# Performance work log

Hardware: AMD Instinct MI355X
Metric: run time of the kernel (lower is better)

The kernel has to match this reference:

```python
import jax, jax.numpy as jnp
import numpy as np

N_NODES = 50000
N_EDGES = 800000
IN_DIM = 128
HID = 128
HEADS = 4
OUT_DIM = 32
NEG_SLOPE = 0.2  # DGL GATConv default


def _gat_params(key, in_dim, out_feat, heads):
    k1, k2, k3 = jax.random.split(key, 3)
    s = 1.0 / np.sqrt(in_dim)
    W = jax.random.normal(k1, (in_dim, heads * out_feat), jnp.float32) * s
    attn_l = jax.random.normal(k2, (heads, out_feat), jnp.float32) * 0.1
    attn_r = jax.random.normal(k3, (heads, out_feat), jnp.float32) * 0.1
    b = jnp.zeros((heads * out_feat,), jnp.float32)
    return W, attn_l, attn_r, b


def setup_inputs() -> dict:
    key = jax.random.key(0)
    ks = jax.random.split(key, 10)
    inp = {
        "x_am": jax.random.normal(ks[0], (N_NODES, IN_DIM), jnp.float32),
        "x_ph": jax.random.normal(ks[1], (N_NODES, IN_DIM), jnp.float32),
        "exist": jax.random.uniform(ks[2], (N_EDGES,), jnp.float32),
        "am_exist": jax.random.uniform(ks[3], (N_EDGES,), jnp.float32),
        "src": jax.random.randint(ks[4], (N_EDGES,), 0, N_NODES, jnp.int32),
        "dst": jax.random.randint(ks[5], (N_EDGES,), 0, N_NODES, jnp.int32),
    }
    # layer 0 (input_dim -> hidden//head per head), layer 1 (hidden -> output_dim per head)
    inp["W0a"], inp["al0a"], inp["ar0a"], inp["b0a"] = _gat_params(ks[6], IN_DIM, HID // HEADS, HEADS)
    inp["W0p"], inp["al0p"], inp["ar0p"], inp["b0p"] = _gat_params(ks[7], IN_DIM, HID // HEADS, HEADS)
    inp["W1a"], inp["al1a"], inp["ar1a"], inp["b1a"] = _gat_params(ks[8], HID, OUT_DIM, HEADS)
    inp["W1p"], inp["al1p"], inp["ar1p"], inp["b1p"] = _gat_params(ks[9], HID, OUT_DIM, HEADS)
    return inp


def gat_conv(x, src, dst, W, attn_l, attn_r, b, edge_w, n_nodes):
    """DGL-style GATConv with edge_weight: out[i] = sum_{e: dst=i} softmax_i(LeakyReLU(el[src]+er[dst])) * w_e * ft[src]."""
    heads, outf = attn_l.shape
    ft = (x @ W).reshape(-1, heads, outf)                 # (N, H, F)
    el = jnp.sum(ft * attn_l, axis=-1)                    # (N, H)
    er = jnp.sum(ft * attn_r, axis=-1)                    # (N, H)
    e = jax.nn.leaky_relu(el[src] + er[dst], NEG_SLOPE)   # (E, H)
    emax = jax.ops.segment_max(e, dst, num_segments=n_nodes)
    emax = jnp.where(jnp.isfinite(emax), emax, 0.0)       # guard isolated nodes
    ex = jnp.exp(e - emax[dst])
    denom = jax.ops.segment_sum(ex, dst, num_segments=n_nodes)
    a = ex / jnp.maximum(denom[dst], 1e-9)                # edge softmax over incoming edges
    a = a * edge_w[:, None]                               # post-softmax edge weighting
    out = jax.ops.segment_sum(ft[src] * a[:, :, None], dst, num_segments=n_nodes)  # (N, H, F)
    return out + b.reshape(heads, outf)


def reference(x_am, x_ph, exist, am_exist,
              W0a, al0a, ar0a, b0a, W0p, al0p, ar0p, b0p,
              W1a, al1a, ar1a, b1a, W1p, al1p, ar1p, b1p,
              src, dst):
    n = x_am.shape[0]
    # layer 0: GATConv -> flatten -> ReLU (dropout rate 0 in eval)
    h_am = gat_conv(x_am, src, dst, W0a, al0a, ar0a, b0a, am_exist, n)
    h_ph = gat_conv(x_ph, src, dst, W0p, al0p, ar0p, b0p, exist, n)
    h_am = jax.nn.relu(h_am.reshape(n, -1))
    h_ph = jax.nn.relu(h_ph.reshape(n, -1))
    # layer 1 (last): GATConv -> mean over heads
    h_am = gat_conv(h_am, src, dst, W1a, al1a, ar1a, b1a, am_exist, n).mean(axis=1)
    h_ph = gat_conv(h_ph, src, dst, W1p, al1p, ar1p, b1p, exist, n).mean(axis=1)
    return (h_am, h_ph)
```

## Files before the change

kernel.cpp:

```cpp
#include <hip/hip_runtime.h>
#include <hip/hip_fp16.h>


typedef _Float16 f16x8 __attribute__((ext_vector_type(8)));
typedef float f32x4 __attribute__((ext_vector_type(4)));

struct GemmP { const void* X; const __half* Wt; const float *al, *ar; __half* Y; float *el, *er; };
struct ChP   { const __half* ft; const float *el, *er, *bias; void* out; };

__global__ void hist_kernel(const int* __restrict__ dst, int* __restrict__ counts, int E) {
  int e = blockIdx.x * blockDim.x + threadIdx.x;
  if (e < E) atomicAdd(&counts[dst[e]], 1);
}

__global__ __launch_bounds__(256) void scan1_kernel(const int* __restrict__ counts,
                                                    int* __restrict__ incl,
                                                    int* __restrict__ bsum, int n) {
  __shared__ int lds[256];
  int i = blockIdx.x * 256 + threadIdx.x;
  int v = (i < n) ? counts[i] : 0;
  lds[threadIdx.x] = v;
  __syncthreads();
  for (int off = 1; off < 256; off <<= 1) {
    int t = (threadIdx.x >= off) ? lds[threadIdx.x - off] : 0;
    __syncthreads();
    lds[threadIdx.x] += t;
    __syncthreads();
  }
  if (i < n) incl[i] = lds[threadIdx.x];
  if (threadIdx.x == 255) bsum[blockIdx.x] = lds[255];
}

__global__ __launch_bounds__(256) void scan2_kernel(int* __restrict__ bsum, int nb) {
  __shared__ int lds[256];
  int carry = 0;
  for (int base = 0; base < nb; base += 256) {
    int i = base + threadIdx.x;
    int v = (i < nb) ? bsum[i] : 0;
    lds[threadIdx.x] = v;
    __syncthreads();
    for (int off = 1; off < 256; off <<= 1) {
      int t = (threadIdx.x >= off) ? lds[threadIdx.x - off] : 0;
      __syncthreads();
      lds[threadIdx.x] += t;
      __syncthreads();
    }
    if (i < nb) bsum[i] = carry + lds[threadIdx.x] - v;
    carry += lds[255];
    __syncthreads();
  }
}

__global__ void scan3_kernel(const int* __restrict__ counts, const int* __restrict__ incl,
                             const int* __restrict__ bsum_ex, int* __restrict__ offsets,
                             int n, int E) {
  int i = blockIdx.x * blockDim.x + threadIdx.x;
  if (i < n) offsets[i] = incl[i] - counts[i] + bsum_ex[i >> 8];
  if (i == 0) offsets[n] = E;
}

__global__ void fill_kernel(const int* __restrict__ src, const int* __restrict__ dst,
                            const float* __restrict__ exist, const float* __restrict__ am_exist,
                            int* __restrict__ cursor, int4* __restrict__ edge16, int E) {
  int e = blockIdx.x * blockDim.x + threadIdx.x;
  if (e >= E) return;
  int pos = atomicAdd(&cursor[dst[e]], 1);
  edge16[pos] = make_int4(src[e], __float_as_int(am_exist[e]), __float_as_int(exist[e]), 0);
}

__global__ void wprep_kernel(const float* __restrict__ W0a, const float* __restrict__ W0p,
                             const float* __restrict__ W1a, const float* __restrict__ W1p,
                             __half* __restrict__ Wt) {
  int m = blockIdx.y;
  const float* W = (m == 0) ? W0a : (m == 1) ? W0p : (m == 2) ? W1a : W1p;
  __half* O = Wt + (size_t)m * 16384;
  int i = blockIdx.x * 256 + threadIdx.x;
  int nn = i >> 7, k = i & 127;
  O[nn * 128 + k] = __float2half_rn(W[k * 128 + nn]);
}

template <int AFP16>
__global__ __launch_bounds__(256) void gemm_kernel(GemmP p0, GemmP p1, int n) {
  GemmP p = blockIdx.y ? p1 : p0;
  constexpr int LDH = 72;
  constexpr int LDE = 136;
  __shared__ __half lds[2 * 128 * LDH];
  __half* As = lds;
  __half* Ws = lds + 128 * LDH;
  int t = threadIdx.x;
  int row0 = blockIdx.x << 7;
  int wv = t >> 6, lane = t & 63;
  int m = lane & 15, q = lane >> 4;

  f32x4 acc[2][8];
#pragma unroll
  for (int rt = 0; rt < 2; ++rt)
#pragma unroll
    for (int ct = 0; ct < 8; ++ct) acc[rt][ct] = (f32x4){0.f, 0.f, 0.f, 0.f};

#pragma unroll
  for (int kh = 0; kh < 2; ++kh) {
    __syncthreads();
    if (AFP16) {
      const __half* Xh = (const __half*)p.X;
#pragma unroll
      for (int i = 0; i < 4; ++i) {
        int c = t + (i << 8);
        int r = c >> 3, o8 = c & 7;
        uint4 v = make_uint4(0, 0, 0, 0);
        if (row0 + r < n)
          v = *(const uint4*)(Xh + (size_t)(row0 + r) * 128 + (kh << 6) + (o8 << 3));
        *(uint4*)(As + r * LDH + (o8 << 3)) = v;
      }
    } else {
      const float* Xf = (const float*)p.X;
#pragma unroll
      for (int i = 0; i < 8; ++i) {
        int c = t + (i << 8);
        int r = c >> 4, f4 = c & 15;
        float4 v = make_float4(0.f, 0.f, 0.f, 0.f);
        if (row0 + r < n)
          v = *(const float4*)(Xf + (size_t)(row0 + r) * 128 + (kh << 6) + (f4 << 2));
        union { __half h[4]; uint2 u; } pk;
        pk.h[0] = __float2half_rn(v.x); pk.h[1] = __float2half_rn(v.y);
        pk.h[2] = __float2half_rn(v.z); pk.h[3] = __float2half_rn(v.w);
        *(uint2*)(As + r * LDH + (f4 << 2)) = pk.u;
      }
    }
#pragma unroll
    for (int i = 0; i < 4; ++i) {
      int c = t + (i << 8);
      int r = c >> 3, o8 = c & 7;
      uint4 v = *(const uint4*)(p.Wt + (size_t)r * 128 + (kh << 6) + (o8 << 3));
      *(uint4*)(Ws + r * LDH + (o8 << 3)) = v;
    }
    __syncthreads();
#pragma unroll
    for (int kc = 0; kc < 2; ++kc) {
      f16x8 a0 = *(const f16x8*)(As + (wv * 32 + m) * LDH + kc * 32 + q * 8);
      f16x8 a1 = *(const f16x8*)(As + (wv * 32 + 16 + m) * LDH + kc * 32 + q * 8);
#pragma unroll
      for (int ct = 0; ct < 8; ++ct) {
        f16x8 b = *(const f16x8*)(Ws + (ct * 16 + m) * LDH + kc * 32 + q * 8);
        acc[0][ct] = __builtin_amdgcn_mfma_f32_16x16x32_f16(a0, b, acc[0][ct], 0, 0, 0);
        acc[1][ct] = __builtin_amdgcn_mfma_f32_16x16x32_f16(a1, b, acc[1][ct], 0, 0, 0);
      }
    }
  }
  __syncthreads();
#pragma unroll
  for (int rt = 0; rt < 2; ++rt) {
    int rbase = wv * 32 + rt * 16 + q * 4;
#pragma unroll
    for (int ct = 0; ct < 8; ++ct) {
      int col = ct * 16 + m;
#pragma unroll
      for (int r = 0; r < 4; ++r)
        lds[(rbase + r) * LDE + col] = __float2half_rn(acc[rt][ct][r]);
    }
  }
  __syncthreads();
  {
    int r = t & 127;
    int half = t >> 7;
    int row = row0 + r;
    if (row < n) {
      float e0 = 0.f, e1 = 0.f, r0 = 0.f, r1 = 0.f;
#pragma unroll
      for (int i = 0; i < 8; ++i) {
        int cbase = half * 64 + i * 8;
        f16x8 v = *(const f16x8*)(lds + r * LDE + cbase);
        *(uint4*)(p.Y + (size_t)row * 128 + cbase) = *(const uint4*)&v;
#pragma unroll
        for (int j = 0; j < 8; ++j) {
          float f = (float)v[j];
          float av = p.al[cbase + j];
          float rv = p.ar[cbase + j];
          if (((i * 8 + j) >> 5) == 0) { e0 = fmaf(f, av, e0); r0 = fmaf(f, rv, r0); }
          else                         { e1 = fmaf(f, av, e1); r1 = fmaf(f, rv, r1); }
        }
      }
      *(float2*)(p.el + (size_t)row * 4 + half * 2) = make_float2(e0, e1);
      *(float2*)(p.er + (size_t)row * 4 + half * 2) = make_float2(r0, r1);
    }
  }
}

template <int LAYER>
__global__ __launch_bounds__(256) void gather_kernel(ChP c0, ChP c1,
                                                     const int* __restrict__ offs,
                                                     const int4* __restrict__ edge16, int n) {
  int t = threadIdx.x;
  int w = t >> 6;
  int lane = t & 63;
  int node = blockIdx.x * 2 + (w >> 1);
  int ch = w & 1;
  if (node >= n) return;
  ChP P = ch ? c1 : c0;
  int hh = lane >> 4;

  int start = __builtin_amdgcn_readfirstlane(offs[node]);
  int end = __builtin_amdgcn_readfirstlane(offs[node + 1]);
  float er_h = P.er[(size_t)node * 4 + hh];
  const __half2* ftbase = (const __half2*)P.ft;
  const float* elbase = P.el;

  float acc0 = 0.f, acc1 = 0.f, l = 0.f;
  int k = start;
  while (k + 8 <= end) {
    int4 ed[8];
#pragma unroll
    for (int j = 0; j < 8; ++j) ed[j] = edge16[k + j];
#pragma unroll
    for (int j = 0; j < 8; ++j) {
      int s = ed[j].x;
      float wgt = __int_as_float(ch ? ed[j].z : ed[j].y);
      float elv = (elbase + (size_t)s * 4)[hh];
      float2 f = __half22float2((ftbase + (size_t)s * 64)[lane]);
      float e = elv + er_h;
      e = (e > 0.f) ? e : 0.2f * e;
      float x = __expf(e);
      l += x;
      float cv = x * wgt;
      acc0 = fmaf(cv, f.x, acc0);
      acc1 = fmaf(cv, f.y, acc1);
    }
    k += 8;
  }
  for (; k < end; ++k) {
    int4 ed = edge16[k];
    int s = ed.x;
    float wgt = __int_as_float(ch ? ed.z : ed.y);
    float elv = (elbase + (size_t)s * 4)[hh];
    float2 f = __half22float2((ftbase + (size_t)s * 64)[lane]);
    float e = elv + er_h;
    e = (e > 0.f) ? e : 0.2f * e;
    float x = __expf(e);
    l += x;
    float cv = x * wgt;
    acc0 = fmaf(cv, f.x, acc0);
    acc1 = fmaf(cv, f.y, acc1);
  }

  float rl = 1.f / fmaxf(l, 1e-9f);
  float2 b2 = *(const float2*)(P.bias + lane * 2);
  float v0 = fmaf(acc0, rl, b2.x);
  float v1 = fmaf(acc1, rl, b2.y);
  if (LAYER == 0) {
    __half2 h = __floats2half2_rn(fmaxf(v0, 0.f), fmaxf(v1, 0.f));
    ((__half2*)P.out)[(size_t)node * 64 + lane] = h;
  } else {
    v0 += __shfl_xor(v0, 16); v1 += __shfl_xor(v1, 16);
    v0 += __shfl_xor(v0, 32); v1 += __shfl_xor(v1, 32);
    if (lane < 16) {
      *(float2*)((float*)P.out + (size_t)node * 32 + lane * 2) =
          make_float2(0.25f * v0, 0.25f * v1);
    }
  }
}

extern "C" void kernel_launch(void* const* d_in, const int* in_sizes, int n_in,
                              void* d_out, int out_size, void* d_ws, size_t ws_size,
                              hipStream_t stream) {
  const float* x_am = (const float*)d_in[0];
  const float* x_ph = (const float*)d_in[1];
  const float* exist = (const float*)d_in[2];
  const float* am_exist = (const float*)d_in[3];
  const int* src = (const int*)d_in[4];
  const int* dst = (const int*)d_in[5];
  const float* W0a = (const float*)d_in[6];
  const float* al0a = (const float*)d_in[7];
  const float* ar0a = (const float*)d_in[8];
  const float* b0a = (const float*)d_in[9];
  const float* W0p = (const float*)d_in[10];
  const float* al0p = (const float*)d_in[11];
  const float* ar0p = (const float*)d_in[12];
  const float* b0p = (const float*)d_in[13];
  const float* W1a = (const float*)d_in[14];
  const float* al1a = (const float*)d_in[15];
  const float* ar1a = (const float*)d_in[16];
  const float* b1a = (const float*)d_in[17];
  const float* W1p = (const float*)d_in[18];
  const float* al1p = (const float*)d_in[19];
  const float* ar1p = (const float*)d_in[20];
  const float* b1p = (const float*)d_in[21];

  int n = in_sizes[0] / 128;
  int E = in_sizes[2];
  int N_pad = (n + 255) & ~255;
  int nb = (n + 255) / 256;
  int NB_pad = (nb + 63) & ~63;

  size_t szN = (size_t)N_pad * 4;
  size_t szOffs = (size_t)(N_pad + 8) * 4;
  size_t szE16 = (size_t)E * 16;
  size_t szFt16 = (size_t)n * 128 * 2;
  size_t szEl = (size_t)N_pad * 4 * 4;
  size_t szWt = (size_t)4 * 128 * 128 * 2;

  auto rnd = [](size_t b) { return (b + 255) & ~(size_t)255; };
  size_t fixed = 3 * rnd(szN) + rnd((size_t)NB_pad * 4) + rnd(szOffs) + rnd(szE16) +
                 4 * rnd(szEl) + rnd(szWt);
  bool dual = ws_size >= fixed + 4 * rnd(szFt16);

  char* p = (char*)d_ws;
  auto take = [&](size_t b) { char* q = p; p += (b + 255) & ~(size_t)255; return q; };
  int* counts = (int*)take(szN);
  int* cursor = (int*)take(szN);
  int* incl = (int*)take(szN);
  int* bsum = (int*)take((size_t)NB_pad * 4);
  int* offs = (int*)take(szOffs);
  int4* edge16 = (int4*)take(szE16);
  __half* Wt = (__half*)take(szWt);
  float* el_am = (float*)take(szEl);
  float* el_ph = (float*)take(szEl);
  float* er_am = (float*)take(szEl);
  float* er_ph = (float*)take(szEl);
  __half* ft_am = (__half*)take(szFt16);
  __half* ft_ph = dual ? (__half*)take(szFt16) : ft_am;
  __half* hb_am = (__half*)take(szFt16);
  __half* hb_ph = dual ? (__half*)take(szFt16) : hb_am;

  float* out_am = (float*)d_out;
  float* out_ph = out_am + (size_t)n * 32;

  hipMemsetAsync(counts, 0, szN, stream);
  hist_kernel<<<(E + 255) / 256, 256, 0, stream>>>(dst, counts, E);
  wprep_kernel<<<dim3(64, 4), 256, 0, stream>>>(W0a, W0p, W1a, W1p, Wt);
  scan1_kernel<<<nb, 256, 0, stream>>>(counts, incl, bsum, n);
  scan2_kernel<<<1, 256, 0, stream>>>(bsum, nb);
  scan3_kernel<<<nb, 256, 0, stream>>>(counts, incl, bsum, offs, n, E);
  hipMemcpyAsync(cursor, offs, szN, hipMemcpyDeviceToDevice, stream);
  fill_kernel<<<(E + 255) / 256, 256, 0, stream>>>(src, dst, exist, am_exist,
                                                   cursor, edge16, E);

  int gg = (n + 127) / 128;
  int gw = (n + 1) / 2;
  GemmP g0a{x_am, Wt,          al0a, ar0a, ft_am, el_am, er_am};
  GemmP g0p{x_ph, Wt + 16384,  al0p, ar0p, ft_ph, el_ph, er_ph};
  GemmP g1a{hb_am, Wt + 32768, al1a, ar1a, ft_am, el_am, er_am};
  GemmP g1p{hb_ph, Wt + 49152, al1p, ar1p, ft_ph, el_ph, er_ph};
  ChP c0a{ft_am, el_am, er_am, b0a, hb_am};
  ChP c0p{ft_ph, el_ph, er_ph, b0p, hb_ph};
  ChP c1a{ft_am, el_am, er_am, b1a, out_am};
  ChP c1p{ft_ph, el_ph, er_ph, b1p, out_ph};

  if (dual) {
    gemm_kernel<0><<<dim3(gg, 2), 256, 0, stream>>>(g0a, g0p, n);
    gather_kernel<0><<<gw, 256, 0, stream>>>(c0a, c0p, offs, edge16, n);
    gemm_kernel<1><<<dim3(gg, 2), 256, 0, stream>>>(g1a, g1p, n);
    gather_kernel<1><<<gw, 256, 0, stream>>>(c1a, c1p, offs, edge16, n);
  } else {
    gemm_kernel<0><<<dim3(gg, 2), 256, 0, stream>>>(g0a, g0a, n);
    gather_kernel<0><<<gw, 256, 0, stream>>>(c0a, c0a, offs, edge16, n);
    gemm_kernel<1><<<dim3(gg, 2), 256, 0, stream>>>(g1a, g1a, n);
    gather_kernel<1><<<gw, 256, 0, stream>>>(c1a, c1a, offs, edge16, n);
    gemm_kernel<0><<<dim3(gg, 2), 256, 0, stream>>>(g0p, g0p, n);
    gather_kernel<0><<<gw, 256, 0, stream>>>(c0p, c0p, offs, edge16, n);
    gemm_kernel<1><<<dim3(gg, 2), 256, 0, stream>>>(g1p, g1p, n);
    gather_kernel<1><<<gw, 256, 0, stream>>>(c1p, c1p, offs, edge16, n);
  }
}
```

Before: 433.8 us.

## Precompute per-edge attention exponentials in a separate edge-parallel kernel

Adds a coef_kernel that, for every CSR-sorted edge, computes exp(leaky_relu(el[src]+er[dst])) for all four heads of both channels and stores them as float4 arrays. The gather kernel then reads these coalesced per-edge values instead of doing a random el[src] load and an exp per lane per edge. To support this, dst is stored in the edge record, and scan3 writes the cursor directly, which removes the device-to-device memcpy. The cost is an extra kernel per layer and about 25 MB of extra write and read traffic for the coefficient arrays.

After: 433.5 us. Within noise of the previous version (-0.1%).

```diff
diff --git a/kernel.cpp b/kernel.cpp
--- a/kernel.cpp
+++ b/kernel.cpp
@@ -6,7 +6,8 @@
 typedef float f32x4 __attribute__((ext_vector_type(4)));
 
 struct GemmP { const void* X; const __half* Wt; const float *al, *ar; __half* Y; float *el, *er; };
-struct ChP   { const __half* ft; const float *el, *er, *bias; void* out; };
+struct ChP   { const __half* ft; const float* X; const float* bias; void* out; };
+struct CoefP { const float *el, *er; float* X; };
 
 __global__ void hist_kernel(const int* __restrict__ dst, int* __restrict__ counts, int E) {
   int e = blockIdx.x * blockDim.x + threadIdx.x;
@@ -53,9 +54,13 @@
 
 __global__ void scan3_kernel(const int* __restrict__ counts, const int* __restrict__ incl,
                              const int* __restrict__ bsum_ex, int* __restrict__ offsets,
-                             int n, int E) {
+                             int* __restrict__ cursor, int n, int E) {
   int i = blockIdx.x * blockDim.x + threadIdx.x;
-  if (i < n) offsets[i] = incl[i] - counts[i] + bsum_ex[i >> 8];
+  if (i < n) {
+    int v = incl[i] - counts[i] + bsum_ex[i >> 8];
+    offsets[i] = v;
+    cursor[i] = v;
+  }
   if (i == 0) offsets[n] = E;
 }
 
@@ -64,8 +69,9 @@
                             int* __restrict__ cursor, int4* __restrict__ edge16, int E) {
   int e = blockIdx.x * blockDim.x + threadIdx.x;
   if (e >= E) return;
-  int pos = atomicAdd(&cursor[dst[e]], 1);
-  edge16[pos] = make_int4(src[e], __float_as_int(am_exist[e]), __float_as_int(exist[e]), 0);
+  int d = dst[e];
+  int pos = atomicAdd(&cursor[d], 1);
+  edge16[pos] = make_int4(src[e], d, __float_as_int(am_exist[e]), __float_as_int(exist[e]));
 }
 
 __global__ void wprep_kernel(const float* __restrict__ W0a, const float* __restrict__ W0p,
@@ -186,6 +192,36 @@
   }
 }
 
+__global__ __launch_bounds__(256) void coef_kernel(CoefP a, CoefP b,
+                                                   const int4* __restrict__ edge16, int E) {
+  int e = blockIdx.x * 256 + threadIdx.x;
+  if (e >= E) return;
+  int4 r = edge16[e];
+  int s = r.x, d = r.y;
+  {
+    float4 el = *(const float4*)(a.el + (size_t)s * 4);
+    float4 er = *(const float4*)(a.er + (size_t)d * 4);
+    float4 x;
+    float v;
+    v = el.x + er.x; v = (v > 0.f) ? v : 0.2f * v; x.x = __expf(v);
+    v = el.y + er.y; v = (v > 0.f) ? v : 0.2f * v; x.y = __expf(v);
+    v = el.z + er.z; v = (v > 0.f) ? v : 0.2f * v; x.z = __expf(v);
+    v = el.w + er.w; v = (v > 0.f) ? v : 0.2f * v; x.w = __expf(v);
+    *(float4*)(a.X + (size_t)e * 4) = x;
+  }
+  {
+    float4 el = *(const float4*)(b.el + (size_t)s * 4);
+    float4 er = *(const float4*)(b.er + (size_t)d * 4);
+    float4 x;
+    float v;
+    v = el.x + er.x; v = (v > 0.f) ? v : 0.2f * v; x.x = __expf(v);
+    v = el.y + er.y; v = (v > 0.f) ? v : 0.2f * v; x.y = __expf(v);
+    v = el.z + er.z; v = (v > 0.f) ? v : 0.2f * v; x.z = __expf(v);
+    v = el.w + er.w; v = (v > 0.f) ? v : 0.2f * v; x.w = __expf(v);
+    *(float4*)(b.X + (size_t)e * 4) = x;
+  }
+}
+
 template <int LAYER>
 __global__ __launch_bounds__(256) void gather_kernel(ChP c0, ChP c1,
                                                      const int* __restrict__ offs,
@@ -201,9 +237,8 @@
 
   int start = __builtin_amdgcn_readfirstlane(offs[node]);
   int end = __builtin_amdgcn_readfirstlane(offs[node + 1]);
-  float er_h = P.er[(size_t)node * 4 + hh];
   const __half2* ftbase = (const __half2*)P.ft;
-  const float* elbase = P.el;
+  const float* Xb = P.X;
 
   float acc0 = 0.f, acc1 = 0.f, l = 0.f;
   int k = start;
@@ -211,35 +246,33 @@
     int4 ed[8];
 #pragma unroll
     for (int j = 0; j < 8; ++j) ed[j] = edge16[k + j];
+    const float* Xk = Xb + (size_t)k * 4;
+    float xs[8];
+#pragma unroll
+    for (int j = 0; j < 8; ++j) xs[j] = Xk[j * 4 + hh];
 #pragma unroll
     for (int j = 0; j < 8; ++j) {
       int s = ed[j].x;
-      float wgt = __int_as_float(ch ? ed[j].z : ed[j].y);
-      float elv = (elbase + (size_t)s * 4)[hh];
-      float2 f = __half22float2((ftbase + (size_t)s * 64)[lane]);
-      float e = elv + er_h;
-      e = (e > 0.f) ? e : 0.2f * e;
-      float x = __expf(e);
+      float wgt = __int_as_float(ch ? ed[j].w : ed[j].z);
+      __half2 fh = ftbase[(size_t)s * 64 + lane];
+      float x = xs[j];
       l += x;
       float cv = x * wgt;
-      acc0 = fmaf(cv, f.x, acc0);
-      acc1 = fmaf(cv, f.y, acc1);
+      acc0 = fmaf(cv, __low2float(fh), acc0);
+      acc1 = fmaf(cv, __high2float(fh), acc1);
     }
     k += 8;
   }
   for (; k < end; ++k) {
     int4 ed = edge16[k];
     int s = ed.x;
-    float wgt = __int_as_float(ch ? ed.z : ed.y);
-    float elv = (elbase + (size_t)s * 4)[hh];
-    float2 f = __half22float2((ftbase + (size_t)s * 64)[lane]);
-    float e = elv + er_h;
-    e = (e > 0.f) ? e : 0.2f * e;
-    float x = __expf(e);
+    float wgt = __int_as_float(ch ? ed.w : ed.z);
+    float x = Xb[(size_t)k * 4 + hh];
+    __half2 fh = ftbase[(size_t)s * 64 + lane];
     l += x;
     float cv = x * wgt;
-    acc0 = fmaf(cv, f.x, acc0);
-    acc1 = fmaf(cv, f.y, acc1);
+    acc0 = fmaf(cv, __low2float(fh), acc0);
+    acc1 = fmaf(cv, __high2float(fh), acc1);
   }
 
   float rl = 1.f / fmaxf(l, 1e-9f);
@@ -297,11 +330,12 @@
   size_t szFt16 = (size_t)n * 128 * 2;
   size_t szEl = (size_t)N_pad * 4 * 4;
   size_t szWt = (size_t)4 * 128 * 128 * 2;
+  size_t szX = (size_t)E * 16;
 
   auto rnd = [](size_t b) { return (b + 255) & ~(size_t)255; };
   size_t fixed = 3 * rnd(szN) + rnd((size_t)NB_pad * 4) + rnd(szOffs) + rnd(szE16) +
-                 4 * rnd(szEl) + rnd(szWt);
-  bool dual = ws_size >= fixed + 4 * rnd(szFt16);
+                 4 * rnd(szEl) + rnd(szWt) + rnd(szX);
+  bool dual = ws_size >= fixed + 4 * rnd(szFt16) + rnd(szX);
 
   char* p = (char*)d_ws;
   auto take = [&](size_t b) { char* q = p; p += (b + 255) & ~(size_t)255; return q; };
@@ -316,6 +350,8 @@
   float* el_ph = (float*)take(szEl);
   float* er_am = (float*)take(szEl);
   float* er_ph = (float*)take(szEl);
+  float* X_am = (float*)take(szX);
+  float* X_ph = dual ? (float*)take(szX) : X_am;
   __half* ft_am = (__half*)take(szFt16);
   __half* ft_ph = dual ? (__half*)take(szFt16) : ft_am;
   __half* hb_am = (__half*)take(szFt16);
@@ -329,35 +365,43 @@
   wprep_kernel<<<dim3(64, 4), 256, 0, stream>>>(W0a, W0p, W1a, W1p, Wt);
   scan1_kernel<<<nb, 256, 0, stream>>>(counts, incl, bsum, n);
   scan2_kernel<<<1, 256, 0, stream>>>(bsum, nb);
-  scan3_kernel<<<nb, 256, 0, stream>>>(counts, incl, bsum, offs, n, E);
-  hipMemcpyAsync(cursor, offs, szN, hipMemcpyDeviceToDevice, stream);
+  scan3_kernel<<<nb, 256, 0, stream>>>(counts, incl, bsum, offs, cursor, n, E);
   fill_kernel<<<(E + 255) / 256, 256, 0, stream>>>(src, dst, exist, am_exist,
                                                    cursor, edge16, E);
 
   int gg = (n + 127) / 128;
   int gw = (n + 1) / 2;
+  int ce = (E + 255) / 256;
   GemmP g0a{x_am, Wt,          al0a, ar0a, ft_am, el_am, er_am};
   GemmP g0p{x_ph, Wt + 16384,  al0p, ar0p, ft_ph, el_ph, er_ph};
   GemmP g1a{hb_am, Wt + 32768, al1a, ar1a, ft_am, el_am, er_am};
   GemmP g1p{hb_ph, Wt + 49152, al1p, ar1p, ft_ph, el_ph, er_ph};
-  ChP c0a{ft_am, el_am, er_am, b0a, hb_am};
-  ChP c0p{ft_ph, el_ph, er_ph, b0p, hb_ph};
-  ChP c1a{ft_am, el_am, er_am, b1a, out_am};
-  ChP c1p{ft_ph, el_ph, er_ph, b1p, out_ph};
+  CoefP ka{el_am, er_am, X_am};
+  CoefP kp{el_ph, er_ph, X_ph};
+  ChP c0a{ft_am, X_am, b0a, hb_am};
+  ChP c0p{ft_ph, X_ph, b0p, hb_ph};
+  ChP c1a{ft_am, X_am, b1a, out_am};
+  ChP c1p{ft_ph, X_ph, b1p, out_ph};
 
   if (dual) {
     gemm_kernel<0><<<dim3(gg, 2), 256, 0, stream>>>(g0a, g0p, n);
+    coef_kernel<<<ce, 256, 0, stream>>>(ka, kp, edge16, E);
     gather_kernel<0><<<gw, 256, 0, stream>>>(c0a, c0p, offs, edge16, n);
     gemm_kernel<1><<<dim3(gg, 2), 256, 0, stream>>>(g1a, g1p, n);
+    coef_kernel<<<ce, 256, 0, stream>>>(ka, kp, edge16, E);
     gather_kernel<1><<<gw, 256, 0, stream>>>(c1a, c1p, offs, edge16, n);
   } else {
     gemm_kernel<0><<<dim3(gg, 2), 256, 0, stream>>>(g0a, g0a, n);
+    coef_kernel<<<ce, 256, 0, stream>>>(ka, ka, edge16, E);
     gather_kernel<0><<<gw, 256, 0, stream>>>(c0a, c0a, offs, edge16, n);
     gemm_kernel<1><<<dim3(gg, 2), 256, 0, stream>>>(g1a, g1a, n);
+    coef_kernel<<<ce, 256, 0, stream>>>(ka, ka, edge16, E);
     gather_kernel<1><<<gw, 256, 0, stream>>>(c1a, c1a, offs, edge16, n);
     gemm_kernel<0><<<dim3(gg, 2), 256, 0, stream>>>(g0p, g0p, n);
+    coef_kernel<<<ce, 256, 0, stream>>>(kp, kp, edge16, E);
     gather_kernel<0><<<gw, 256, 0, stream>>>(c0p, c0p, offs, edge16, n);
     gemm_kernel<1><<<dim3(gg, 2), 256, 0, stream>>>(g1p, g1p, n);
+    coef_kernel<<<ce, 256, 0, stream>>>(kp, kp, edge16, E);
     gather_kernel<1><<<gw, 256, 0, stream>>>(c1p, c1p, offs, edge16, n);
   }
 }
```
